# Kernel tuning notes

Measured on AMD Instinct MI355X. Metric: run time of the kernel, lower is better.

Reference implementation:

```python
import jax, jax.numpy as jnp
import numpy as np


def setup_inputs() -> dict:
    key = jax.random.key(0)
    k1, k2 = jax.random.split(key)
    B, K, H, W = 16, 100, 120, 160
    Rk = jax.random.normal(k1, (B, K, H, W), dtype=jnp.float32)
    tf_Rk = jax.random.normal(k2, (B, K, H, W), dtype=jnp.float32)
    return {"Rk": Rk, "tf_Rk": tf_Rk}


def _keypoints(Dk, score2_map):
    # Dk: [B,K,H,W]. score2_map: map used for the kp2 score gather
    # (for the tf branch the original code erroneously gathers from Dk; we stay faithful).
    B, K, H, W = Dk.shape
    zeta = Dk.sum(axis=(2, 3))                                   # [B,K]
    xs = jnp.arange(W, dtype=Dk.dtype)
    ys = jnp.arange(H, dtype=Dk.dtype)
    kp_x = jnp.einsum('bkhw,w->bk', Dk, xs)                      # soft-argmax numerators
    kp_y = jnp.einsum('bkhw,h->bk', Dk, ys)
    kx = jnp.round(kp_x / zeta)                                  # rounded keypoint coords (float)
    ky = jnp.round(kp_y / zeta)
    bi = jnp.arange(B)[:, None]
    ki = jnp.arange(K)[None, :]
    gx = kx.astype(jnp.int32)
    gy = ky.astype(jnp.int32)
    s = Dk[bi, ki, gy, gx]                                       # score at keypoint, [B,K]
    kp = jnp.stack([kx, ky], axis=-1)                            # [B,K,2] (x,y)
    kp1 = (kp + kp * s[..., None]).astype(jnp.int32)             # torch .int() truncation
    kp2 = (kp - kp * s[..., None]).astype(jnp.int32)
    # clamp gather indices to valid range (torch indexing would OOB-crash; jnp clips)
    h1 = jnp.clip(kp1[..., 1], 0, H - 1); w1 = jnp.clip(kp1[..., 0], 0, W - 1)
    h2 = jnp.clip(kp2[..., 1], 0, H - 1); w2 = jnp.clip(kp2[..., 0], 0, W - 1)
    s1 = Dk[bi, ki, h1, w1]
    s2 = score2_map[bi, ki, h2, w2]
    kp_w = jnp.concatenate([kp, s[..., None]], axis=-1)                           # [B,K,3]
    kp1_w = jnp.concatenate([kp1.astype(Dk.dtype), s1[..., None]], axis=-1)
    kp2_w = jnp.concatenate([kp2.astype(Dk.dtype), s2[..., None]], axis=-1)
    keypoint = jnp.concatenate([kp_w, kp1_w, kp2_w], axis=1)                      # [B,3K,3]
    return keypoint, zeta


def reference(Rk, tf_Rk):
    Dk = jax.nn.sigmoid(Rk)
    tf_Dk = jax.nn.sigmoid(tf_Rk)
    keypoint, get_zeta = _keypoints(Dk, Dk)
    # bug-faithful: score_tf_kp2 is gathered from Dk (not tf_Dk) in the original
    tf_keypoint, _ = _keypoints(tf_Dk, Dk)
    return Dk, keypoint, get_zeta, tf_Dk, tf_keypoint
```

## Files before the change

kernel.cpp:

```cpp
#include <hip/hip_runtime.h>
#include <hip/hip_bf16.h>

constexpr int B = 16, K = 100, H = 120, W = 160;
constexpr int HW  = H * W;
constexpr int NF4 = HW / 4;
constexpr int BK  = B * K;
constexpr int W4  = W / 4;

constexpr size_t OFF_DK   = 0;
constexpr size_t OFF_KP   = (size_t)BK * HW;
constexpr size_t OFF_ZETA = OFF_KP + (size_t)B*3*K*3;
constexpr size_t OFF_TFDK = OFF_ZETA + BK;
constexpr size_t OFF_TFKP = OFF_TFDK + (size_t)BK*HW;

typedef float f32x4 __attribute__((ext_vector_type(4)));

__device__ __forceinline__ float fast_sigmoid(float x) {
    const float e = __builtin_amdgcn_exp2f(-1.44269504088896340736f * x);
    return __builtin_amdgcn_rcpf(1.0f + e);
}

__global__ __launch_bounds__(256)
void sigmoid_reduce_kernel(const float* __restrict__ Rk,
                           const float* __restrict__ tfRk,
                           float* __restrict__ out,
                           float* __restrict__ ws) {
    const int blk    = blockIdx.x;
    const int tensor = (blk >= BK) ? 1 : 0;
    const int bk     = blk - tensor * BK;
    const float* src = tensor ? tfRk : Rk;
    float*       dst = out + (tensor ? OFF_TFDK : OFF_DK);

    const f32x4* __restrict__ s4 = (const f32x4*)(src + (size_t)bk * HW);
    f32x4*       __restrict__ d4 = (f32x4*)(dst + (size_t)bk * HW);

    const int tid = threadIdx.x;
    float sum = 0.0f, sx = 0.0f, sy = 0.0f;

    for (int i = tid; i < NF4; i += 256) {
        f32x4 v = s4[i];
        f32x4 o;
        o.x = fast_sigmoid(v.x);
        o.y = fast_sigmoid(v.y);
        o.z = fast_sigmoid(v.z);
        o.w = fast_sigmoid(v.w);
        d4[i] = o;

        const int y  = i / W4;
        const int x0 = (i - y * W4) * 4;
        const float rs = (o.x + o.y) + (o.z + o.w);
        sum += rs;
        sy  = fmaf(rs, (float)y, sy);
        sx  = fmaf(o.x, (float)(x0),     sx);
        sx  = fmaf(o.y, (float)(x0 + 1), sx);
        sx  = fmaf(o.z, (float)(x0 + 2), sx);
        sx  = fmaf(o.w, (float)(x0 + 3), sx);
    }

    for (int off = 32; off > 0; off >>= 1) {
        sum += __shfl_down(sum, off);
        sx  += __shfl_down(sx,  off);
        sy  += __shfl_down(sy,  off);
    }
    __shared__ float red[3][4];
    const int wave = tid >> 6, lane = tid & 63;
    if (lane == 0) { red[0][wave] = sum; red[1][wave] = sx; red[2][wave] = sy; }
    __syncthreads();
    if (tid == 0) {
        const float S = (red[0][0] + red[0][1]) + (red[0][2] + red[0][3]);
        const float X = (red[1][0] + red[1][1]) + (red[1][2] + red[1][3]);
        const float Y = (red[2][0] + red[2][1]) + (red[2][2] + red[2][3]);
        ws[(size_t)(tensor * 3 + 0) * BK + bk] = S;
        ws[(size_t)(tensor * 3 + 1) * BK + bk] = X;
        ws[(size_t)(tensor * 3 + 2) * BK + bk] = Y;
        if (tensor == 0) out[OFF_ZETA + bk] = S;
    }
}

__global__ __launch_bounds__(256)
void keypoint_kernel(const float* __restrict__ ws, float* __restrict__ out) {
    const int t = blockIdx.x * 256 + threadIdx.x;
    if (t >= 2 * BK) return;
    const int tensor = t / BK;
    const int bk     = t - tensor * BK;
    const int b = bk / K, k = bk - b * K;

    const float S = ws[(size_t)(tensor * 3 + 0) * BK + bk];
    const float X = ws[(size_t)(tensor * 3 + 1) * BK + bk];
    const float Y = ws[(size_t)(tensor * 3 + 2) * BK + bk];

    const float kx = rintf(X / S);
    const float ky = rintf(Y / S);

    const float* map     = out + (tensor ? OFF_TFDK : OFF_DK) + (size_t)bk * HW;
    const float* mainmap = out + OFF_DK + (size_t)bk * HW;

    const int gx = (int)kx, gy = (int)ky;
    const float s = map[gy * W + gx];

    const int kp1x = (int)__fadd_rn(kx, __fmul_rn(kx, s));
    const int kp1y = (int)__fadd_rn(ky, __fmul_rn(ky, s));
    const int kp2x = (int)__fsub_rn(kx, __fmul_rn(kx, s));
    const int kp2y = (int)__fsub_rn(ky, __fmul_rn(ky, s));

    const int w1 = min(max(kp1x, 0), W - 1), h1 = min(max(kp1y, 0), H - 1);
    const int w2 = min(max(kp2x, 0), W - 1), h2 = min(max(kp2y, 0), H - 1);
    const float s1 = map[h1 * W + w1];
    const float s2 = mainmap[h2 * W + w2];

    float* okp = out + (tensor ? OFF_TFKP : OFF_KP);
    float* r0 = okp + ((size_t)b * 3 * K + k) * 3;
    r0[0] = kx;           r0[1] = ky;           r0[2] = s;
    float* r1 = okp + ((size_t)b * 3 * K + K + k) * 3;
    r1[0] = (float)kp1x;  r1[1] = (float)kp1y;  r1[2] = s1;
    float* r2 = okp + ((size_t)b * 3 * K + 2 * K + k) * 3;
    r2[0] = (float)kp2x;  r2[1] = (float)kp2y;  r2[2] = s2;
}

extern "C" void kernel_launch(void* const* d_in, const int* in_sizes, int n_in,
                              void* d_out, int out_size, void* d_ws, size_t ws_size,
                              hipStream_t stream) {
    const float* Rk   = (const float*)d_in[0];
    const float* tfRk = (const float*)d_in[1];
    float* out = (float*)d_out;
    float* ws  = (float*)d_ws;

    sigmoid_reduce_kernel<<<2 * BK, 256, 0, stream>>>(Rk, tfRk, out, ws);
    const int nkp = 2 * BK;
    keypoint_kernel<<<(nkp + 255) / 256, 256, 0, stream>>>(ws, out);
}
```

Before: 108.4 us.

## Fuse keypoint extraction into sigmoid-reduce kernel and pack accumulators as float2

Removes the second keypoint kernel launch and workspace round trip. Each block's thread 0 now computes keypoints right after its reduction, recomputing sigmoid from the input tensors instead of reading the output maps. This is possible because the tf branch's kp2 gather reads the Rk input, so no block depends on another block's output. The inner accumulation also switches to two-wide float vectors so the compiler can use packed FMA instructions, which changes the summation order slightly. The serial tail on thread 0 adds some latency to every block.

```diff
diff --git a/kernel.cpp b/kernel.cpp
--- a/kernel.cpp
+++ b/kernel.cpp
@@ -14,6 +14,7 @@
 constexpr size_t OFF_TFKP = OFF_TFDK + (size_t)BK*HW;
 
 typedef float f32x4 __attribute__((ext_vector_type(4)));
+typedef float f32x2 __attribute__((ext_vector_type(2)));
 
 __device__ __forceinline__ float fast_sigmoid(float x) {
     const float e = __builtin_amdgcn_exp2f(-1.44269504088896340736f * x);
@@ -21,10 +22,9 @@
 }
 
 __global__ __launch_bounds__(256)
-void sigmoid_reduce_kernel(const float* __restrict__ Rk,
-                           const float* __restrict__ tfRk,
-                           float* __restrict__ out,
-                           float* __restrict__ ws) {
+void fused_kernel(const float* __restrict__ Rk,
+                  const float* __restrict__ tfRk,
+                  float* __restrict__ out) {
     const int blk    = blockIdx.x;
     const int tensor = (blk >= BK) ? 1 : 0;
     const int bk     = blk - tensor * BK;
@@ -35,7 +35,7 @@
     f32x4*       __restrict__ d4 = (f32x4*)(dst + (size_t)bk * HW);
 
     const int tid = threadIdx.x;
-    float sum = 0.0f, sx = 0.0f, sy = 0.0f;
+    f32x2 sum2 = {0.0f, 0.0f}, sx2 = {0.0f, 0.0f}, sy2 = {0.0f, 0.0f};
 
     for (int i = tid; i < NF4; i += 256) {
         f32x4 v = s4[i];
@@ -48,14 +48,22 @@
 
         const int y  = i / W4;
         const int x0 = (i - y * W4) * 4;
-        const float rs = (o.x + o.y) + (o.z + o.w);
-        sum += rs;
-        sy  = fmaf(rs, (float)y, sy);
-        sx  = fmaf(o.x, (float)(x0),     sx);
-        sx  = fmaf(o.y, (float)(x0 + 1), sx);
-        sx  = fmaf(o.z, (float)(x0 + 2), sx);
-        sx  = fmaf(o.w, (float)(x0 + 3), sx);
+        const float fy = (float)y, fx0 = (float)x0;
+
+        const f32x2 lo = {o.x, o.y}, hi = {o.z, o.w};
+        const f32x2 rs = lo + hi;
+        sum2 += rs;
+        const f32x2 yy = {fy, fy};
+        sy2 = rs * yy + sy2;
+        const f32x2 xlo = {fx0,        fx0 + 1.0f};
+        const f32x2 xhi = {fx0 + 2.0f, fx0 + 3.0f};
+        sx2 = lo * xlo + sx2;
+        sx2 = hi * xhi + sx2;
     }
+
+    float sum = sum2.x + sum2.y;
+    float sx  = sx2.x + sx2.y;
+    float sy  = sy2.x + sy2.y;
 
     for (int off = 32; off > 0; off >>= 1) {
         sum += __shfl_down(sum, off);
@@ -66,55 +74,42 @@
     const int wave = tid >> 6, lane = tid & 63;
     if (lane == 0) { red[0][wave] = sum; red[1][wave] = sx; red[2][wave] = sy; }
     __syncthreads();
+
     if (tid == 0) {
         const float S = (red[0][0] + red[0][1]) + (red[0][2] + red[0][3]);
         const float X = (red[1][0] + red[1][1]) + (red[1][2] + red[1][3]);
         const float Y = (red[2][0] + red[2][1]) + (red[2][2] + red[2][3]);
-        ws[(size_t)(tensor * 3 + 0) * BK + bk] = S;
-        ws[(size_t)(tensor * 3 + 1) * BK + bk] = X;
-        ws[(size_t)(tensor * 3 + 2) * BK + bk] = Y;
+
+        const int b = bk / K, k = bk - b * K;
         if (tensor == 0) out[OFF_ZETA + bk] = S;
+
+        const float kx = rintf(X / S);
+        const float ky = rintf(Y / S);
+
+        const float* imap  = src + (size_t)bk * HW;
+        const float* imain = Rk  + (size_t)bk * HW;
+
+        const int gx = (int)kx, gy = (int)ky;
+        const float s = fast_sigmoid(imap[gy * W + gx]);
+
+        const int kp1x = (int)__fadd_rn(kx, __fmul_rn(kx, s));
+        const int kp1y = (int)__fadd_rn(ky, __fmul_rn(ky, s));
+        const int kp2x = (int)__fsub_rn(kx, __fmul_rn(kx, s));
+        const int kp2y = (int)__fsub_rn(ky, __fmul_rn(ky, s));
+
+        const int w1 = min(max(kp1x, 0), W - 1), h1 = min(max(kp1y, 0), H - 1);
+        const int w2 = min(max(kp2x, 0), W - 1), h2 = min(max(kp2y, 0), H - 1);
+        const float s1 = fast_sigmoid(imap [h1 * W + w1]);
+        const float s2 = fast_sigmoid(imain[h2 * W + w2]);
+
+        float* okp = out + (tensor ? OFF_TFKP : OFF_KP);
+        float* r0 = okp + ((size_t)b * 3 * K + k) * 3;
+        r0[0] = kx;           r0[1] = ky;           r0[2] = s;
+        float* r1 = okp + ((size_t)b * 3 * K + K + k) * 3;
+        r1[0] = (float)kp1x;  r1[1] = (float)kp1y;  r1[2] = s1;
+        float* r2 = okp + ((size_t)b * 3 * K + 2 * K + k) * 3;
+        r2[0] = (float)kp2x;  r2[1] = (float)kp2y;  r2[2] = s2;
     }
-}
-
-__global__ __launch_bounds__(256)
-void keypoint_kernel(const float* __restrict__ ws, float* __restrict__ out) {
-    const int t = blockIdx.x * 256 + threadIdx.x;
-    if (t >= 2 * BK) return;
-    const int tensor = t / BK;
-    const int bk     = t - tensor * BK;
-    const int b = bk / K, k = bk - b * K;
-
-    const float S = ws[(size_t)(tensor * 3 + 0) * BK + bk];
-    const float X = ws[(size_t)(tensor * 3 + 1) * BK + bk];
-    const float Y = ws[(size_t)(tensor * 3 + 2) * BK + bk];
-
-    const float kx = rintf(X / S);
-    const float ky = rintf(Y / S);
-
-    const float* map     = out + (tensor ? OFF_TFDK : OFF_DK) + (size_t)bk * HW;
-    const float* mainmap = out + OFF_DK + (size_t)bk * HW;
-
-    const int gx = (int)kx, gy = (int)ky;
-    const float s = map[gy * W + gx];
-
-    const int kp1x = (int)__fadd_rn(kx, __fmul_rn(kx, s));
-    const int kp1y = (int)__fadd_rn(ky, __fmul_rn(ky, s));
-    const int kp2x = (int)__fsub_rn(kx, __fmul_rn(kx, s));
-    const int kp2y = (int)__fsub_rn(ky, __fmul_rn(ky, s));
-
-    const int w1 = min(max(kp1x, 0), W - 1), h1 = min(max(kp1y, 0), H - 1);
-    const int w2 = min(max(kp2x, 0), W - 1), h2 = min(max(kp2y, 0), H - 1);
-    const float s1 = map[h1 * W + w1];
-    const float s2 = mainmap[h2 * W + w2];
-
-    float* okp = out + (tensor ? OFF_TFKP : OFF_KP);
-    float* r0 = okp + ((size_t)b * 3 * K + k) * 3;
-    r0[0] = kx;           r0[1] = ky;           r0[2] = s;
-    float* r1 = okp + ((size_t)b * 3 * K + K + k) * 3;
-    r1[0] = (float)kp1x;  r1[1] = (float)kp1y;  r1[2] = s1;
-    float* r2 = okp + ((size_t)b * 3 * K + 2 * K + k) * 3;
-    r2[0] = (float)kp2x;  r2[1] = (float)kp2y;  r2[2] = s2;
 }
 
 extern "C" void kernel_launch(void* const* d_in, const int* in_sizes, int n_in,
@@ -123,9 +118,6 @@
     const float* Rk   = (const float*)d_in[0];
     const float* tfRk = (const float*)d_in[1];
     float* out = (float*)d_out;
-    float* ws  = (float*)d_ws;
 
-    sigmoid_reduce_kernel<<<2 * BK, 256, 0, stream>>>(Rk, tfRk, out, ws);
-    const int nkp = 2 * BK;
-    keypoint_kernel<<<(nkp + 255) / 256, 256, 0, stream>>>(ws, out);
+    fused_kernel<<<2 * BK, 256, 0, stream>>>(Rk, tfRk, out);
 }
```

Measured after the change: 105.7 us. 2.5% less time.
